# Performance work log

Hardware: AMD Instinct MI355X
Metric: run time of the kernel (lower is better)

## Reference

```python
import jax, jax.numpy as jnp
import numpy as np

N_NODES = 100000
N_EDGES = 1600000
IN_CH, HID1, HID2, HID3, OUT_CH = 128, 64, 64, 256, 64


def gcn_conv(x, W, b, src, dst, n_nodes):
    """PyG GCNConv: linear transform, add self-loops, symmetric-normalized aggregation."""
    h = x @ W  # [N, d_out]
    # degree at target nodes, counting the self-loop (+1)
    deg = jnp.zeros((n_nodes,), dtype=h.dtype).at[dst].add(1.0) + 1.0
    dinv = jax.lax.rsqrt(deg)  # deg >= 1, safe
    norm = dinv[src] * dinv[dst]  # [E]
    # scatter-add normalized messages from src to dst
    agg = jnp.zeros_like(h).at[dst].add(h[src] * norm[:, None])
    # self-loop contribution: norm_ii = dinv[i]^2
    agg = agg + h * (dinv * dinv)[:, None]
    return agg + b


def setup_inputs() -> dict:
    key = jax.random.key(0)
    ks = jax.random.split(key, 8)
    x = jax.random.normal(ks[0], (N_NODES, IN_CH), dtype=jnp.float32)
    edge_index = jax.random.randint(ks[1], (2, N_EDGES), 0, N_NODES, dtype=jnp.int64)
    def glorot(k, fan_in, fan_out):
        s = jnp.sqrt(6.0 / (fan_in + fan_out)).astype(jnp.float32)
        return jax.random.uniform(k, (fan_in, fan_out), jnp.float32, -s, s)
    return {
        "x": x,
        "edge_index": edge_index,
        "W1": glorot(ks[2], IN_CH, HID1), "b1": jnp.zeros((HID1,), jnp.float32),
        "W2": glorot(ks[3], HID1, HID2), "b2": jnp.zeros((HID2,), jnp.float32),
        "W3": glorot(ks[4], HID2, HID3), "b3": jnp.zeros((HID3,), jnp.float32),
        "W4": glorot(ks[5], HID3, OUT_CH), "b4": jnp.zeros((OUT_CH,), jnp.float32),
    }


def reference(x, edge_index, W1, b1, W2, b2, W3, b3, W4, b4):
    src, dst = edge_index[0], edge_index[1]
    n = x.shape[0]
    h = jax.nn.relu(gcn_conv(x, W1, b1, src, dst, n))
    h = jax.nn.relu(gcn_conv(h, W2, b2, src, dst, n))
    h = h @ W3 + b3  # hidden Linear (no activation, per original forward)
    h = h @ W4 + b4  # output Linear
    return jax.nn.log_softmax(h, axis=-1)
```

## Files before the change

kernel.cpp:

```cpp
#include <hip/hip_runtime.h>
#include <hip/hip_bf16.h>
#include <math.h>

#define NNODES 100000
#define NEDGES 1600000
#define NB 782
#define PB 256
#define EPB 6250
#define SCAN_N (NB * PB)
#define SB ((SCAN_N + 1023) / 1024)
#define CAP 4608
#define HTS 72
#define ANB 64

typedef __bf16 bf16x8 __attribute__((ext_vector_type(8)));
typedef float f32x4 __attribute__((ext_vector_type(4)));
typedef unsigned int u32x4 __attribute__((ext_vector_type(4)));
typedef unsigned short u16x8 __attribute__((ext_vector_type(8)));

static __device__ inline unsigned short f2bf(float f) {
    __hip_bfloat16 h = __float2bfloat16(f);
    return *reinterpret_cast<unsigned short*>(&h);
}


static __device__ inline int packidx64(int k, int ch) {
    int s = k >> 5, r5 = k & 31, q = r5 >> 3, ii = r5 & 7;
    int t = ch >> 4, lo = ch & 15;
    int lane = q * 16 + lo;
    return ((t * 2 + s) * 64 + lane) * 8 + ii;
}

__global__ __launch_bounds__(256) void histprep_kernel(const int* __restrict__ dst,
                                                       int* __restrict__ histg,
                                                       const float* __restrict__ W1,
                                                       const float* __restrict__ W2,
                                                       const float* __restrict__ W3,
                                                       const float* __restrict__ W4,
                                                       const float* __restrict__ b3,
                                                       const float* __restrict__ b4,
                                                       unsigned short* __restrict__ Wp1,
                                                       unsigned short* __restrict__ Wp2,
                                                       unsigned short* __restrict__ Wp34,
                                                       float* __restrict__ b34,
                                                       unsigned short* __restrict__ hp) {
    __shared__ int h[NB];
    int tid = threadIdx.x, blk = blockIdx.x;
    if (blk < PB) {
        for (int b = tid; b < NB; b += 256) h[b] = 0;
        __syncthreads();
        int base = blk * EPB;
        for (int i = base + tid; i < base + EPB; i += 256)
            atomicAdd(&h[dst[i] >> 7], 1);
        __syncthreads();
        for (int b = tid; b < NB; b += 256) histg[b * PB + blk] = h[b];
        return;
    }
    int pb = blk - PB;
    if (pb < 32) {
        int idx = pb * 256 + tid;
        int i = idx & 7, rest = idx >> 3;
        int lane = rest & 63; rest >>= 6;
        int s = rest % 4, t = rest / 4;
        int k = s * 32 + (lane >> 4) * 8 + i;
        int ch = t * 16 + (lane & 15);
        Wp1[idx] = f2bf(W1[k * 64 + ch]);
    } else if (pb < 48) {
        int idx = (pb - 32) * 256 + tid;
        int i = idx & 7, rest = idx >> 3;
        int lane = rest & 63; rest >>= 6;
        int s = rest % 2, t = rest / 2;
        int k = s * 32 + (lane >> 4) * 8 + i;
        int ch = t * 16 + (lane & 15);
        Wp2[idx] = f2bf(W2[k * 64 + ch]);
    } else if (pb == 48) {
        if (tid < 64) hp[(size_t)NNODES * 64 + tid] = 0;
    } else if (pb < 65) {
        int i = (pb - 49) * 4 + (tid >> 6);
        int j = tid & 63;
        float a = 0.f;
        for (int k = 0; k < 256; ++k) a = fmaf(W3[i * 256 + k], W4[k * 64 + j], a);
        Wp34[packidx64(i, j)] = f2bf(a);
    } else {
        if (tid < 64) {
            int j = tid;
            float a = b4[j];
            for (int k = 0; k < 256; ++k) a = fmaf(b3[k], W4[k * 64 + j], a);
            b34[j] = a;
        }
    }
}


__global__ __launch_bounds__(256) void scan1_kernel(const int* __restrict__ cnt,
                                                    int* __restrict__ off,
                                                    int* __restrict__ bsum, int n) {
    __shared__ int tmp[256];
    int tid = threadIdx.x;
    int t4 = blockIdx.x * 1024 + tid * 4;
    int v0 = (t4 + 0 < n) ? cnt[t4 + 0] : 0;
    int v1 = (t4 + 1 < n) ? cnt[t4 + 1] : 0;
    int v2 = (t4 + 2 < n) ? cnt[t4 + 2] : 0;
    int v3 = (t4 + 3 < n) ? cnt[t4 + 3] : 0;
    int ssum = v0 + v1 + v2 + v3;
    tmp[tid] = ssum;
    __syncthreads();
    for (int d = 1; d < 256; d <<= 1) {
        int x = (tid >= d) ? tmp[tid - d] : 0;
        __syncthreads();
        tmp[tid] += x;
        __syncthreads();
    }
    int run = tmp[tid] - ssum;
    if (t4 + 0 < n) off[t4 + 0] = run; run += v0;
    if (t4 + 1 < n) off[t4 + 1] = run; run += v1;
    if (t4 + 2 < n) off[t4 + 2] = run; run += v2;
    if (t4 + 3 < n) off[t4 + 3] = run;
    if (tid == 255) bsum[blockIdx.x] = tmp[255];
}


__global__ __launch_bounds__(256) void part_kernel(const int* __restrict__ src,
                                                   const int* __restrict__ dst,
                                                   const int* __restrict__ histg,
                                                   const int* __restrict__ gscan,
                                                   const int* __restrict__ bsum,
                                                   unsigned int* __restrict__ part) {
    __shared__ unsigned int sorted[EPB];
    __shared__ int gaddr[EPB];
    __shared__ int gcol[NB];
    __shared__ int base_l[NB];
    __shared__ int cur[NB];
    __shared__ int tmp[256];
    __shared__ int bse[256];
    int tid = threadIdx.x, blk = blockIdx.x;
    int bv = (tid < SB) ? bsum[tid] : 0;
    tmp[tid] = bv;
    __syncthreads();
    for (int d = 1; d < 256; d <<= 1) {
        int x = (tid >= d) ? tmp[tid - d] : 0;
        __syncthreads();
        tmp[tid] += x;
        __syncthreads();
    }
    bse[tid] = tmp[tid] - bv;
    __syncthreads();
    for (int b = tid; b < NB; b += 256) {
        int i = b * PB + blk;
        gcol[b] = gscan[i] + bse[i >> 10];
        base_l[b] = histg[i];
        cur[b] = 0;
    }
    __syncthreads();
    int t4 = tid * 4;
    int v0 = (t4 + 0 < NB) ? base_l[t4 + 0] : 0;
    int v1 = (t4 + 1 < NB) ? base_l[t4 + 1] : 0;
    int v2 = (t4 + 2 < NB) ? base_l[t4 + 2] : 0;
    int v3 = (t4 + 3 < NB) ? base_l[t4 + 3] : 0;
    int ssum = v0 + v1 + v2 + v3;
    tmp[tid] = ssum;
    __syncthreads();
    for (int d = 1; d < 256; d <<= 1) {
        int x = (tid >= d) ? tmp[tid - d] : 0;
        __syncthreads();
        tmp[tid] += x;
        __syncthreads();
    }
    int run = tmp[tid] - ssum;
    if (t4 + 0 < NB) base_l[t4 + 0] = run; run += v0;
    if (t4 + 1 < NB) base_l[t4 + 1] = run; run += v1;
    if (t4 + 2 < NB) base_l[t4 + 2] = run; run += v2;
    if (t4 + 3 < NB) base_l[t4 + 3] = run;
    __syncthreads();
    int base = blk * EPB;
    for (int i = base + tid; i < base + EPB; i += 256) {
        int s = src[i], d = dst[i];
        int bkt = d >> 7;
        int r = atomicAdd(&cur[bkt], 1);
        int pos = base_l[bkt] + r;
        sorted[pos] = ((unsigned int)(d & 127) << 17) | (unsigned int)s;
        gaddr[pos] = gcol[bkt] + r;
    }
    __syncthreads();
    for (int i = tid; i < EPB; i += 256)
        part[gaddr[i]] = sorted[i];
}


__global__ __launch_bounds__(256) void csrgemm_kernel(const unsigned int* __restrict__ part,
                                                      const int* __restrict__ gscan,
                                                      const int* __restrict__ bsum,
                                                      const float* __restrict__ x,
                                                      const unsigned short* __restrict__ Wp1,
                                                      int* __restrict__ csr,
                                                      int* __restrict__ cnt_g,
                                                      int* __restrict__ off_g,
                                                      float* __restrict__ dinv_g,
                                                      unsigned short* __restrict__ hp, int n) {
    __shared__ unsigned int stage[CAP];
    __shared__ int hist2[128];
    __shared__ int sc[128];
    __shared__ int excl[128];
    __shared__ int cur2[128];
    __shared__ float sdinv[128];
    __shared__ int tmp[256];
    __shared__ int bse[256];
    int tid = threadIdx.x, b = blockIdx.x;
    int bv = (tid < SB) ? bsum[tid] : 0;
    tmp[tid] = bv;
    __syncthreads();
    for (int d = 1; d < 256; d <<= 1) {
        int x2 = (tid >= d) ? tmp[tid - d] : 0;
        __syncthreads();
        tmp[tid] += x2;
        __syncthreads();
    }
    bse[tid] = tmp[tid] - bv;
    __syncthreads();
    int i0 = b * PB;
    int S = gscan[i0] + bse[i0 >> 10];
    int T = (b == NB - 1) ? NEDGES : (gscan[i0 + PB] + bse[(i0 + PB) >> 10]);
    int len = T - S;
    bool fit = (len <= CAP);
    if (tid < 128) { hist2[tid] = 0; cur2[tid] = 0; }
    __syncthreads();
    for (int i = tid; i < len; i += 256) {
        unsigned int p = part[S + i];
        if (fit) stage[i] = p;
        atomicAdd(&hist2[p >> 17], 1);
    }
    __syncthreads();
    if (tid < 128) sc[tid] = hist2[tid];
    __syncthreads();
    for (int d = 1; d < 128; d <<= 1) {
        int x2 = 0;
        if (tid < 128 && tid >= d) x2 = sc[tid - d];
        __syncthreads();
        if (tid < 128) sc[tid] += x2;
        __syncthreads();
    }
    if (tid < 128) {
        int c = hist2[tid];
        int ex = sc[tid] - c;
        excl[tid] = ex;
        float dv = rsqrtf((float)c + 1.0f);
        sdinv[tid] = dv;
        int node = b * 128 + tid;
        if (node < n) {
            cnt_g[node] = c;
            off_g[node] = S + ex;
            dinv_g[node] = dv;
        }
    }
    __syncthreads();
    for (int i = tid; i < len; i += 256) {
        unsigned int p = fit ? stage[i] : part[S + i];
        int dl = p >> 17;
        int s = (int)(p & 0x1FFFFu);
        int r = atomicAdd(&cur2[dl], 1);
        csr[S + excl[dl] + r] = s;
    }
    int wv = tid >> 6, lane = tid & 63;
    int q = lane >> 4, lo = lane & 15;
#pragma unroll
    for (int t2 = 0; t2 < 2; ++t2) {
        int nl0 = wv * 32 + t2 * 16;
        int nodeA = b * 128 + nl0 + lo;
        int na = nodeA < n ? nodeA : 0;
        f32x4 acc[4] = {};
#pragma unroll
        for (int s = 0; s < 4; ++s) {
            const float* xr = x + (size_t)na * 128 + q * 8 + s * 32;
            float4 u = *(const float4*)(xr);
            float4 v = *(const float4*)(xr + 4);
            bf16x8 a;
            a[0] = (__bf16)u.x; a[1] = (__bf16)u.y; a[2] = (__bf16)u.z; a[3] = (__bf16)u.w;
            a[4] = (__bf16)v.x; a[5] = (__bf16)v.y; a[6] = (__bf16)v.z; a[7] = (__bf16)v.w;
#pragma unroll
            for (int t = 0; t < 4; ++t) {
                bf16x8 bfr = *(const bf16x8*)(Wp1 + ((size_t)(t * 4 + s) * 64 + lane) * 8);
                acc[t] = __builtin_amdgcn_mfma_f32_16x16x32_bf16(a, bfr, acc[t], 0, 0, 0);
            }
        }
#pragma unroll
        for (int r = 0; r < 4; ++r) {
            int nl = nl0 + q * 4 + r;
            int node = b * 128 + nl;
            if (node < n) {
                float di = sdinv[nl];
#pragma unroll
                for (int t = 0; t < 4; ++t)
                    hp[(size_t)node * 64 + t * 16 + lo] = f2bf(acc[t][r] * di);
            }
        }
    }
}


template <bool LSM>
__global__ __launch_bounds__(256) void aggfuse_kernel(const unsigned short* __restrict__ hsrc,
                                                      const int* __restrict__ csr,
                                                      const int* __restrict__ off,
                                                      const int* __restrict__ cnt,
                                                      const float* __restrict__ dinv,
                                                      const float* __restrict__ biasA,
                                                      const unsigned short* __restrict__ Wp,
                                                      const float* __restrict__ biasB,
                                                      unsigned short* __restrict__ outb,
                                                      float* __restrict__ outf, int n) {
    __shared__ __align__(16) unsigned short ht[ANB * HTS];
    int tid = threadIdx.x, b = blockIdx.x;
    int g = tid >> 3, cl = tid & 7, c8 = cl * 8;
    float4 bv0 = *(const float4*)(biasA + c8);
    float4 bv1 = *(const float4*)(biasA + c8 + 4);
    float bb[8] = {bv0.x, bv0.y, bv0.z, bv0.w, bv1.x, bv1.y, bv1.z, bv1.w};
#pragma unroll 1
    for (int i = 0; i < 2; ++i) {
        int nl = g * 2 + i;
        int node = b * ANB + nl;
        u16x8 hv;
#pragma unroll
        for (int k = 0; k < 8; ++k) hv[k] = 0;
        if (node < n) {
            int s = off[node];
            int c = cnt[node];
            const int* cp = csr + s;
            float acc0[8];
            float acc1[8] = {};
            bf16x8 sv = *(const bf16x8*)(hsrc + (size_t)node * 64 + c8);
            u32x4 su = __builtin_bit_cast(u32x4, sv);
#pragma unroll
            for (int k = 0; k < 4; ++k) {
                acc0[2 * k]     = __builtin_bit_cast(float, su[k] << 16);
                acc0[2 * k + 1] = __builtin_bit_cast(float, su[k] & 0xFFFF0000u);
            }
            int n0 = 0, n1 = 0, n2 = 0, n3 = 0;
            if (c >= 4) { n0 = cp[0]; n1 = cp[1]; n2 = cp[2]; n3 = cp[3]; }
            int j = 0;
            for (; j + 4 <= c; j += 4) {
                bf16x8 va = *(const bf16x8*)(hsrc + (size_t)n0 * 64 + c8);
                bf16x8 vb = *(const bf16x8*)(hsrc + (size_t)n1 * 64 + c8);
                bf16x8 vc = *(const bf16x8*)(hsrc + (size_t)n2 * 64 + c8);
                bf16x8 vd = *(const bf16x8*)(hsrc + (size_t)n3 * 64 + c8);
                int jn = j + 4;
                if (jn + 4 <= c) { n0 = cp[jn]; n1 = cp[jn + 1]; n2 = cp[jn + 2]; n3 = cp[jn + 3]; }
                u32x4 ua = __builtin_bit_cast(u32x4, va);
                u32x4 ub = __builtin_bit_cast(u32x4, vb);
                u32x4 uc = __builtin_bit_cast(u32x4, vc);
                u32x4 ud = __builtin_bit_cast(u32x4, vd);
#pragma unroll
                for (int k = 0; k < 4; ++k) {
                    acc0[2 * k]     += __builtin_bit_cast(float, ua[k] << 16);
                    acc0[2 * k + 1] += __builtin_bit_cast(float, ua[k] & 0xFFFF0000u);
                    acc1[2 * k]     += __builtin_bit_cast(float, ub[k] << 16);
                    acc1[2 * k + 1] += __builtin_bit_cast(float, ub[k] & 0xFFFF0000u);
                    acc0[2 * k]     += __builtin_bit_cast(float, uc[k] << 16);
                    acc0[2 * k + 1] += __builtin_bit_cast(float, uc[k] & 0xFFFF0000u);
                    acc1[2 * k]     += __builtin_bit_cast(float, ud[k] << 16);
                    acc1[2 * k + 1] += __builtin_bit_cast(float, ud[k] & 0xFFFF0000u);
                }
            }
            for (; j < c; ++j) {
                int nt = cp[j];
                bf16x8 va = *(const bf16x8*)(hsrc + (size_t)nt * 64 + c8);
                u32x4 ua = __builtin_bit_cast(u32x4, va);
#pragma unroll
                for (int k = 0; k < 4; ++k) {
                    acc0[2 * k]     += __builtin_bit_cast(float, ua[k] << 16);
                    acc0[2 * k + 1] += __builtin_bit_cast(float, ua[k] & 0xFFFF0000u);
                }
            }
            float di = dinv[node];
#pragma unroll
            for (int k = 0; k < 8; ++k)
                hv[k] = f2bf(fmaxf(fmaf(acc0[k] + acc1[k], di, bb[k]), 0.f));
        }
        *(u16x8*)(&ht[nl * HTS + c8]) = hv;
    }
    __syncthreads();
    int wv = tid >> 6, lane = tid & 63;
    int q = lane >> 4, lo = lane & 15;
    int nl0 = wv * 16;
    f32x4 acc[4] = {};
#pragma unroll
    for (int s = 0; s < 2; ++s) {
        bf16x8 a = *(const bf16x8*)(&ht[(nl0 + lo) * HTS + s * 32 + q * 8]);
#pragma unroll
        for (int t = 0; t < 4; ++t) {
            bf16x8 bfr = *(const bf16x8*)(Wp + ((size_t)(t * 2 + s) * 64 + lane) * 8);
            acc[t] = __builtin_amdgcn_mfma_f32_16x16x32_bf16(a, bfr, acc[t], 0, 0, 0);
        }
    }
    if (!LSM) {
#pragma unroll
        for (int r = 0; r < 4; ++r) {
            int node = b * ANB + nl0 + q * 4 + r;
            if (node < n) {
                float di = dinv[node];
#pragma unroll
                for (int t = 0; t < 4; ++t)
                    outb[(size_t)node * 64 + t * 16 + lo] = f2bf(acc[t][r] * di);
            }
        }
    } else {
#pragma unroll
        for (int r = 0; r < 4; ++r) {
            int node = b * ANB + nl0 + q * 4 + r;
            float v0 = acc[0][r] + biasB[0 * 16 + lo];
            float v1 = acc[1][r] + biasB[1 * 16 + lo];
            float v2 = acc[2][r] + biasB[2 * 16 + lo];
            float v3 = acc[3][r] + biasB[3 * 16 + lo];
            float mx = fmaxf(fmaxf(v0, v1), fmaxf(v2, v3));
            for (int d = 1; d < 16; d <<= 1) mx = fmaxf(mx, __shfl_xor(mx, d));
            float sm = __expf(v0 - mx) + __expf(v1 - mx) + __expf(v2 - mx) + __expf(v3 - mx);
            for (int d = 1; d < 16; d <<= 1) sm += __shfl_xor(sm, d);
            float lse = mx + __logf(sm);
            if (node < n) {
                outf[(size_t)node * 64 + 0 * 16 + lo] = v0 - lse;
                outf[(size_t)node * 64 + 1 * 16 + lo] = v1 - lse;
                outf[(size_t)node * 64 + 2 * 16 + lo] = v2 - lse;
                outf[(size_t)node * 64 + 3 * 16 + lo] = v3 - lse;
            }
        }
    }
}


extern "C" void kernel_launch(void* const* d_in, const int* in_sizes, int n_in,
                              void* d_out, int out_size, void* d_ws, size_t ws_size,
                              hipStream_t stream) {
    const float* x  = (const float*)d_in[0];
    const int*   ei = (const int*)d_in[1];
    const float* W1 = (const float*)d_in[2];
    const float* b1 = (const float*)d_in[3];
    const float* W2 = (const float*)d_in[4];
    const float* b2 = (const float*)d_in[5];
    const float* W3 = (const float*)d_in[6];
    const float* b3 = (const float*)d_in[7];
    const float* W4 = (const float*)d_in[8];
    const float* b4 = (const float*)d_in[9];
    float* outp = (float*)d_out;

    const int N = NNODES;
    const int E = NEDGES;
    const int* srcp = ei;
    const int* dstp = ei + E;

    char* w = (char*)d_ws;
    size_t o = 0;
    auto alloc = [&](size_t bytes) { size_t r = o; o = (o + bytes + 255) & ~(size_t)255; return r; };
    size_t cnt_off   = alloc((size_t)N * 4);
    size_t off_off   = alloc((size_t)N * 4);
    size_t dinv_off  = alloc((size_t)N * 4);
    size_t histg_off = alloc((size_t)SCAN_N * 4);
    size_t gscan_off = alloc((size_t)SCAN_N * 4);
    size_t bs_off    = alloc(256 * 4);
    size_t part_off  = alloc((size_t)E * 4);
    size_t csr_off   = alloc((size_t)E * 4);
    size_t hp_off    = alloc((size_t)(N + 1) * 64 * 2);
    size_t abf_off   = alloc((size_t)N * 64 * 2);
    size_t wp1_off   = alloc(128 * 64 * 2);
    size_t wp2_off   = alloc(64 * 64 * 2);
    size_t wp34_off  = alloc(64 * 64 * 2);
    size_t b34_off   = alloc(64 * 4);

    int*            cnt   = (int*)(w + cnt_off);
    int*            off   = (int*)(w + off_off);
    float*          dinv  = (float*)(w + dinv_off);
    int*            histg = (int*)(w + histg_off);
    int*            gscan = (int*)(w + gscan_off);
    int*            bs    = (int*)(w + bs_off);
    unsigned int*   part  = (unsigned int*)(w + part_off);
    int*            csr   = (int*)(w + csr_off);
    unsigned short* hp    = (unsigned short*)(w + hp_off);
    unsigned short* abf   = (unsigned short*)(w + abf_off);
    unsigned short* Wp1   = (unsigned short*)(w + wp1_off);
    unsigned short* Wp2   = (unsigned short*)(w + wp2_off);
    unsigned short* Wp34  = (unsigned short*)(w + wp34_off);
    float*          b34   = (float*)(w + b34_off);

    histprep_kernel<<<PB + 66, 256, 0, stream>>>(dstp, histg, W1, W2, W3, W4, b3, b4,
                                                 Wp1, Wp2, Wp34, b34, hp);
    scan1_kernel<<<SB, 256, 0, stream>>>(histg, gscan, bs, SCAN_N);
    part_kernel<<<PB, 256, 0, stream>>>(srcp, dstp, histg, gscan, bs, part);
    csrgemm_kernel<<<NB, 256, 0, stream>>>(part, gscan, bs, x, Wp1, csr, cnt, off, dinv, hp, N);

    const int ab = (N + ANB - 1) / ANB;

    aggfuse_kernel<false><<<ab, 256, 0, stream>>>(hp, csr, off, cnt, dinv, b1, Wp2,
                                                  nullptr, abf, nullptr, N);
    aggfuse_kernel<true><<<ab, 256, 0, stream>>>(abf, csr, off, cnt, dinv, b2, Wp34,
                                                 b34, nullptr, outp, N);
}
```

Before: 245.0 us.

## Split fused aggregate-GEMM into column-sliced aggregation and separate GEMM kernels

```diff
diff --git a/kernel.cpp b/kernel.cpp
--- a/kernel.cpp
+++ b/kernel.cpp
@@ -10,13 +10,11 @@
 #define SCAN_N (NB * PB)
 #define SB ((SCAN_N + 1023) / 1024)
 #define CAP 4608
-#define HTS 72
-#define ANB 64
+#define NCH 391
 
 typedef __bf16 bf16x8 __attribute__((ext_vector_type(8)));
 typedef float f32x4 __attribute__((ext_vector_type(4)));
 typedef unsigned int u32x4 __attribute__((ext_vector_type(4)));
-typedef unsigned short u16x8 __attribute__((ext_vector_type(8)));
 
 static __device__ inline unsigned short f2bf(float f) {
     __hip_bfloat16 h = __float2bfloat16(f);
@@ -297,104 +295,100 @@
 }
 
 
+__global__ __launch_bounds__(256) void aggslice_kernel(const unsigned short* __restrict__ hsrc,
+                                                       const int* __restrict__ csr,
+                                                       const int* __restrict__ off,
+                                                       const int* __restrict__ cnt,
+                                                       const float* __restrict__ dinv,
+                                                       const float* __restrict__ bias,
+                                                       unsigned short* __restrict__ out, int n) {
+    int bid = blockIdx.x;
+    int chunk = bid >> 3, slice8 = (bid & 7) * 8;
+    int node = chunk * 256 + threadIdx.x;
+    if (node >= n) return;
+    const unsigned short* tab = hsrc + slice8;
+
+    int c = cnt[node];
+    int s = off[node];
+    const int* cp = csr + s;
+
+    float accA[8];
+    float accB[8] = {};
+    {
+        u32x4 su = *(const u32x4*)(tab + (size_t)node * 64);
+#pragma unroll
+        for (int k = 0; k < 4; ++k) {
+            accA[2 * k]     = __builtin_bit_cast(float, su[k] << 16);
+            accA[2 * k + 1] = __builtin_bit_cast(float, su[k] & 0xFFFF0000u);
+        }
+    }
+    int s0 = 0, s1 = 0;
+    if (c > 0) s0 = cp[0];
+    if (c > 1) s1 = cp[1];
+    int j = 0;
+    for (; j + 2 <= c; j += 2) {
+        u32x4 ua = *(const u32x4*)(tab + (size_t)s0 * 64);
+        u32x4 ub = *(const u32x4*)(tab + (size_t)s1 * 64);
+        if (j + 3 < c)      { s0 = cp[j + 2]; s1 = cp[j + 3]; }
+        else if (j + 2 < c) { s0 = cp[j + 2]; }
+#pragma unroll
+        for (int k = 0; k < 4; ++k) {
+            accA[2 * k]     += __builtin_bit_cast(float, ua[k] << 16);
+            accA[2 * k + 1] += __builtin_bit_cast(float, ua[k] & 0xFFFF0000u);
+            accB[2 * k]     += __builtin_bit_cast(float, ub[k] << 16);
+            accB[2 * k + 1] += __builtin_bit_cast(float, ub[k] & 0xFFFF0000u);
+        }
+    }
+    if (j < c) {
+        u32x4 ua = *(const u32x4*)(tab + (size_t)s0 * 64);
+#pragma unroll
+        for (int k = 0; k < 4; ++k) {
+            accA[2 * k]     += __builtin_bit_cast(float, ua[k] << 16);
+            accA[2 * k + 1] += __builtin_bit_cast(float, ua[k] & 0xFFFF0000u);
+        }
+    }
+
+    float di = dinv[node];
+    float4 bv0 = *(const float4*)(bias + slice8);
+    float4 bv1 = *(const float4*)(bias + slice8 + 4);
+    float bb[8] = {bv0.x, bv0.y, bv0.z, bv0.w, bv1.x, bv1.y, bv1.z, bv1.w};
+    unsigned short ov[8];
+#pragma unroll
+    for (int k = 0; k < 8; ++k)
+        ov[k] = f2bf(fmaxf(fmaf(accA[k] + accB[k], di, bb[k]), 0.f));
+    *(ushort4*)(out + (size_t)node * 64 + slice8)     = make_ushort4(ov[0], ov[1], ov[2], ov[3]);
+    *(ushort4*)(out + (size_t)node * 64 + slice8 + 4) = make_ushort4(ov[4], ov[5], ov[6], ov[7]);
+}
+
+
 template <bool LSM>
-__global__ __launch_bounds__(256) void aggfuse_kernel(const unsigned short* __restrict__ hsrc,
-                                                      const int* __restrict__ csr,
-                                                      const int* __restrict__ off,
-                                                      const int* __restrict__ cnt,
-                                                      const float* __restrict__ dinv,
-                                                      const float* __restrict__ biasA,
-                                                      const unsigned short* __restrict__ Wp,
-                                                      const float* __restrict__ biasB,
-                                                      unsigned short* __restrict__ outb,
-                                                      float* __restrict__ outf, int n) {
-    __shared__ __align__(16) unsigned short ht[ANB * HTS];
-    int tid = threadIdx.x, b = blockIdx.x;
-    int g = tid >> 3, cl = tid & 7, c8 = cl * 8;
-    float4 bv0 = *(const float4*)(biasA + c8);
-    float4 bv1 = *(const float4*)(biasA + c8 + 4);
-    float bb[8] = {bv0.x, bv0.y, bv0.z, bv0.w, bv1.x, bv1.y, bv1.z, bv1.w};
-#pragma unroll 1
-    for (int i = 0; i < 2; ++i) {
-        int nl = g * 2 + i;
-        int node = b * ANB + nl;
-        u16x8 hv;
-#pragma unroll
-        for (int k = 0; k < 8; ++k) hv[k] = 0;
-        if (node < n) {
-            int s = off[node];
-            int c = cnt[node];
-            const int* cp = csr + s;
-            float acc0[8];
-            float acc1[8] = {};
-            bf16x8 sv = *(const bf16x8*)(hsrc + (size_t)node * 64 + c8);
-            u32x4 su = __builtin_bit_cast(u32x4, sv);
-#pragma unroll
-            for (int k = 0; k < 4; ++k) {
-                acc0[2 * k]     = __builtin_bit_cast(float, su[k] << 16);
-                acc0[2 * k + 1] = __builtin_bit_cast(float, su[k] & 0xFFFF0000u);
-            }
-            int n0 = 0, n1 = 0, n2 = 0, n3 = 0;
-            if (c >= 4) { n0 = cp[0]; n1 = cp[1]; n2 = cp[2]; n3 = cp[3]; }
-            int j = 0;
-            for (; j + 4 <= c; j += 4) {
-                bf16x8 va = *(const bf16x8*)(hsrc + (size_t)n0 * 64 + c8);
-                bf16x8 vb = *(const bf16x8*)(hsrc + (size_t)n1 * 64 + c8);
-                bf16x8 vc = *(const bf16x8*)(hsrc + (size_t)n2 * 64 + c8);
-                bf16x8 vd = *(const bf16x8*)(hsrc + (size_t)n3 * 64 + c8);
-                int jn = j + 4;
-                if (jn + 4 <= c) { n0 = cp[jn]; n1 = cp[jn + 1]; n2 = cp[jn + 2]; n3 = cp[jn + 3]; }
-                u32x4 ua = __builtin_bit_cast(u32x4, va);
-                u32x4 ub = __builtin_bit_cast(u32x4, vb);
-                u32x4 uc = __builtin_bit_cast(u32x4, vc);
-                u32x4 ud = __builtin_bit_cast(u32x4, vd);
-#pragma unroll
-                for (int k = 0; k < 4; ++k) {
-                    acc0[2 * k]     += __builtin_bit_cast(float, ua[k] << 16);
-                    acc0[2 * k + 1] += __builtin_bit_cast(float, ua[k] & 0xFFFF0000u);
-                    acc1[2 * k]     += __builtin_bit_cast(float, ub[k] << 16);
-                    acc1[2 * k + 1] += __builtin_bit_cast(float, ub[k] & 0xFFFF0000u);
-                    acc0[2 * k]     += __builtin_bit_cast(float, uc[k] << 16);
-                    acc0[2 * k + 1] += __builtin_bit_cast(float, uc[k] & 0xFFFF0000u);
-                    acc1[2 * k]     += __builtin_bit_cast(float, ud[k] << 16);
-                    acc1[2 * k + 1] += __builtin_bit_cast(float, ud[k] & 0xFFFF0000u);
-                }
-            }
-            for (; j < c; ++j) {
-                int nt = cp[j];
-                bf16x8 va = *(const bf16x8*)(hsrc + (size_t)nt * 64 + c8);
-                u32x4 ua = __builtin_bit_cast(u32x4, va);
-#pragma unroll
-                for (int k = 0; k < 4; ++k) {
-                    acc0[2 * k]     += __builtin_bit_cast(float, ua[k] << 16);
-                    acc0[2 * k + 1] += __builtin_bit_cast(float, ua[k] & 0xFFFF0000u);
-                }
-            }
-            float di = dinv[node];
-#pragma unroll
-            for (int k = 0; k < 8; ++k)
-                hv[k] = f2bf(fmaxf(fmaf(acc0[k] + acc1[k], di, bb[k]), 0.f));
-        }
-        *(u16x8*)(&ht[nl * HTS + c8]) = hv;
-    }
-    __syncthreads();
-    int wv = tid >> 6, lane = tid & 63;
+__global__ __launch_bounds__(256) void gemm64_kernel(const unsigned short* __restrict__ Xb,
+                                                     const unsigned short* __restrict__ Wp,
+                                                     const float* __restrict__ biasB,
+                                                     const float* __restrict__ dinv,
+                                                     unsigned short* __restrict__ outb,
+                                                     float* __restrict__ outf, int n) {
+    int w = threadIdx.x >> 6, lane = threadIdx.x & 63;
     int q = lane >> 4, lo = lane & 15;
-    int nl0 = wv * 16;
+    int base = blockIdx.x * 64 + w * 16;
+    int nodeA = base + lo;
+    int na = nodeA < n ? nodeA : 0;
+
     f32x4 acc[4] = {};
 #pragma unroll
     for (int s = 0; s < 2; ++s) {
-        bf16x8 a = *(const bf16x8*)(&ht[(nl0 + lo) * HTS + s * 32 + q * 8]);
+        bf16x8 a = *(const bf16x8*)(Xb + (size_t)na * 64 + q * 8 + s * 32);
 #pragma unroll
         for (int t = 0; t < 4; ++t) {
-            bf16x8 bfr = *(const bf16x8*)(Wp + ((size_t)(t * 2 + s) * 64 + lane) * 8);
-            acc[t] = __builtin_amdgcn_mfma_f32_16x16x32_bf16(a, bfr, acc[t], 0, 0, 0);
-        }
-    }
+            bf16x8 b = *(const bf16x8*)(Wp + ((size_t)(t * 2 + s) * 64 + lane) * 8);
+            acc[t] = __builtin_amdgcn_mfma_f32_16x16x32_bf16(a, b, acc[t], 0, 0, 0);
+        }
+    }
+
     if (!LSM) {
 #pragma unroll
         for (int r = 0; r < 4; ++r) {
-            int node = b * ANB + nl0 + q * 4 + r;
+            int node = base + q * 4 + r;
             if (node < n) {
                 float di = dinv[node];
 #pragma unroll
@@ -405,7 +399,7 @@
     } else {
 #pragma unroll
         for (int r = 0; r < 4; ++r) {
-            int node = b * ANB + nl0 + q * 4 + r;
+            int node = base + q * 4 + r;
             float v0 = acc[0][r] + biasB[0 * 16 + lo];
             float v1 = acc[1][r] + biasB[1 * 16 + lo];
             float v2 = acc[2][r] + biasB[2 * 16 + lo];
@@ -485,10 +479,11 @@
     part_kernel<<<PB, 256, 0, stream>>>(srcp, dstp, histg, gscan, bs, part);
     csrgemm_kernel<<<NB, 256, 0, stream>>>(part, gscan, bs, x, Wp1, csr, cnt, off, dinv, hp, N);
 
-    const int ab = (N + ANB - 1) / ANB;
-
-    aggfuse_kernel<false><<<ab, 256, 0, stream>>>(hp, csr, off, cnt, dinv, b1, Wp2,
-                                                  nullptr, abf, nullptr, N);
-    aggfuse_kernel<true><<<ab, 256, 0, stream>>>(abf, csr, off, cnt, dinv, b2, Wp34,
-                                                 b34, nullptr, outp, N);
-}
+    const int ag = NCH * 8;
+    const int gb = (N + 63) / 64;
+
+    aggslice_kernel<<<ag, 256, 0, stream>>>(hp, csr, off, cnt, dinv, b1, abf, N);
+    gemm64_kernel<false><<<gb, 256, 0, stream>>>(abf, Wp2, nullptr, dinv, hp, nullptr, N);
+    aggslice_kernel<<<ag, 256, 0, stream>>>(hp, csr, off, cnt, dinv, b2, abf, N);
+    gemm64_kernel<true><<<gb, 256, 0, stream>>>(abf, Wp34, b34, nullptr, nullptr, outp, N);
+}
```

Result: slower. 664.1 us (+171.1%).

## Sort nodes by degree so aggregation blocks get balanced neighbor counts

Applied to the files above, without the earlier changes.

```diff
diff --git a/kernel.cpp b/kernel.cpp
--- a/kernel.cpp
+++ b/kernel.cpp
@@ -12,6 +12,7 @@
 #define CAP 4608
 #define HTS 72
 #define ANB 64
+#define DBINS 64
 
 typedef __bf16 bf16x8 __attribute__((ext_vector_type(8)));
 typedef float f32x4 __attribute__((ext_vector_type(4)));
@@ -43,7 +44,9 @@
                                                        unsigned short* __restrict__ Wp2,
                                                        unsigned short* __restrict__ Wp34,
                                                        float* __restrict__ b34,
-                                                       unsigned short* __restrict__ hp) {
+                                                       unsigned short* __restrict__ hp,
+                                                       int* __restrict__ dhist,
+                                                       int* __restrict__ gcur) {
     __shared__ int h[NB];
     int tid = threadIdx.x, blk = blockIdx.x;
     if (blk < PB) {
@@ -75,6 +78,7 @@
         Wp2[idx] = f2bf(W2[k * 64 + ch]);
     } else if (pb == 48) {
         if (tid < 64) hp[(size_t)NNODES * 64 + tid] = 0;
+        if (tid < DBINS) { dhist[tid] = 0; gcur[tid] = 0; }
     } else if (pb < 65) {
         int i = (pb - 49) * 4 + (tid >> 6);
         int j = tid & 63;
@@ -127,7 +131,7 @@
                                                    const int* __restrict__ bsum,
                                                    unsigned int* __restrict__ part) {
     __shared__ unsigned int sorted[EPB];
-    __shared__ int gaddr[EPB];
+    __shared__ unsigned short bktb[EPB];
     __shared__ int gcol[NB];
     __shared__ int base_l[NB];
     __shared__ int cur[NB];
@@ -179,11 +183,13 @@
         int r = atomicAdd(&cur[bkt], 1);
         int pos = base_l[bkt] + r;
         sorted[pos] = ((unsigned int)(d & 127) << 17) | (unsigned int)s;
-        gaddr[pos] = gcol[bkt] + r;
-    }
-    __syncthreads();
-    for (int i = tid; i < EPB; i += 256)
-        part[gaddr[i]] = sorted[i];
+        bktb[pos] = (unsigned short)bkt;
+    }
+    __syncthreads();
+    for (int i = tid; i < EPB; i += 256) {
+        int bkt = bktb[i];
+        part[gcol[bkt] + (i - base_l[bkt])] = sorted[i];
+    }
 }
 
 
@@ -196,7 +202,8 @@
                                                       int* __restrict__ cnt_g,
                                                       int* __restrict__ off_g,
                                                       float* __restrict__ dinv_g,
-                                                      unsigned short* __restrict__ hp, int n) {
+                                                      unsigned short* __restrict__ hp,
+                                                      int* __restrict__ dhist, int n) {
     __shared__ unsigned int stage[CAP];
     __shared__ int hist2[128];
     __shared__ int sc[128];
@@ -205,6 +212,7 @@
     __shared__ float sdinv[128];
     __shared__ int tmp[256];
     __shared__ int bse[256];
+    __shared__ int dh[DBINS];
     int tid = threadIdx.x, b = blockIdx.x;
     int bv = (tid < SB) ? bsum[tid] : 0;
     tmp[tid] = bv;
@@ -223,6 +231,7 @@
     int len = T - S;
     bool fit = (len <= CAP);
     if (tid < 128) { hist2[tid] = 0; cur2[tid] = 0; }
+    if (tid < DBINS) dh[tid] = 0;
     __syncthreads();
     for (int i = tid; i < len; i += 256) {
         unsigned int p = part[S + i];
@@ -250,9 +259,11 @@
             cnt_g[node] = c;
             off_g[node] = S + ex;
             dinv_g[node] = dv;
-        }
-    }
-    __syncthreads();
+            atomicAdd(&dh[c < 63 ? c : 63], 1);
+        }
+    }
+    __syncthreads();
+    if (tid < DBINS && dh[tid] > 0) atomicAdd(&dhist[tid], dh[tid]);
     for (int i = tid; i < len; i += 256) {
         unsigned int p = fit ? stage[i] : part[S + i];
         int dl = p >> 17;
@@ -293,6 +304,44 @@
                     hp[(size_t)node * 64 + t * 16 + lo] = f2bf(acc[t][r] * di);
             }
         }
+    }
+}
+
+
+__global__ __launch_bounds__(256) void permute_kernel(const int* __restrict__ cnt,
+                                                      const int* __restrict__ dhist,
+                                                      int* __restrict__ gcur,
+                                                      int* __restrict__ perm, int n) {
+    __shared__ int dbase[DBINS];
+    __shared__ int lh[DBINS];
+    __shared__ int lbase[DBINS];
+    __shared__ int lcur[DBINS];
+    __shared__ int sc[DBINS];
+    int tid = threadIdx.x;
+    int node = blockIdx.x * 256 + tid;
+    if (tid < DBINS) { sc[tid] = dhist[tid]; lh[tid] = 0; lcur[tid] = 0; }
+    __syncthreads();
+    for (int d = 1; d < DBINS; d <<= 1) {
+        int v = 0;
+        if (tid < DBINS && tid >= d) v = sc[tid - d];
+        __syncthreads();
+        if (tid < DBINS) sc[tid] += v;
+        __syncthreads();
+    }
+    if (tid < DBINS) dbase[tid] = sc[tid] - dhist[tid];
+    __syncthreads();
+    int bin = -1;
+    if (node < n) {
+        int c = cnt[node];
+        bin = c < 63 ? c : 63;
+        atomicAdd(&lh[bin], 1);
+    }
+    __syncthreads();
+    if (tid < DBINS && lh[tid] > 0) lbase[tid] = atomicAdd(&gcur[tid], lh[tid]);
+    __syncthreads();
+    if (node < n) {
+        int r = atomicAdd(&lcur[bin], 1);
+        perm[dbase[bin] + lbase[bin] + r] = node;
     }
 }
 
@@ -306,9 +355,11 @@
                                                       const float* __restrict__ biasA,
                                                       const unsigned short* __restrict__ Wp,
                                                       const float* __restrict__ biasB,
+                                                      const int* __restrict__ perm,
                                                       unsigned short* __restrict__ outb,
                                                       float* __restrict__ outf, int n) {
     __shared__ __align__(16) unsigned short ht[ANB * HTS];
+    __shared__ int pnode[ANB];
     int tid = threadIdx.x, b = blockIdx.x;
     int g = tid >> 3, cl = tid & 7, c8 = cl * 8;
     float4 bv0 = *(const float4*)(biasA + c8);
@@ -317,11 +368,13 @@
 #pragma unroll 1
     for (int i = 0; i < 2; ++i) {
         int nl = g * 2 + i;
-        int node = b * ANB + nl;
+        int slot = b * ANB + nl;
+        int node = (slot < n) ? perm[slot] : -1;
+        if (cl == 0) pnode[nl] = node;
         u16x8 hv;
 #pragma unroll
         for (int k = 0; k < 8; ++k) hv[k] = 0;
-        if (node < n) {
+        if (node >= 0) {
             int s = off[node];
             int c = cnt[node];
             const int* cp = csr + s;
@@ -394,8 +447,8 @@
     if (!LSM) {
 #pragma unroll
         for (int r = 0; r < 4; ++r) {
-            int node = b * ANB + nl0 + q * 4 + r;
-            if (node < n) {
+            int node = pnode[nl0 + q * 4 + r];
+            if (node >= 0) {
                 float di = dinv[node];
 #pragma unroll
                 for (int t = 0; t < 4; ++t)
@@ -405,7 +458,7 @@
     } else {
 #pragma unroll
         for (int r = 0; r < 4; ++r) {
-            int node = b * ANB + nl0 + q * 4 + r;
+            int node = pnode[nl0 + q * 4 + r];
             float v0 = acc[0][r] + biasB[0 * 16 + lo];
             float v1 = acc[1][r] + biasB[1 * 16 + lo];
             float v2 = acc[2][r] + biasB[2 * 16 + lo];
@@ -415,7 +468,7 @@
             float sm = __expf(v0 - mx) + __expf(v1 - mx) + __expf(v2 - mx) + __expf(v3 - mx);
             for (int d = 1; d < 16; d <<= 1) sm += __shfl_xor(sm, d);
             float lse = mx + __logf(sm);
-            if (node < n) {
+            if (node >= 0) {
                 outf[(size_t)node * 64 + 0 * 16 + lo] = v0 - lse;
                 outf[(size_t)node * 64 + 1 * 16 + lo] = v1 - lse;
                 outf[(size_t)node * 64 + 2 * 16 + lo] = v2 - lse;
@@ -452,9 +505,12 @@
     size_t cnt_off   = alloc((size_t)N * 4);
     size_t off_off   = alloc((size_t)N * 4);
     size_t dinv_off  = alloc((size_t)N * 4);
+    size_t perm_off  = alloc((size_t)N * 4);
     size_t histg_off = alloc((size_t)SCAN_N * 4);
     size_t gscan_off = alloc((size_t)SCAN_N * 4);
     size_t bs_off    = alloc(256 * 4);
+    size_t dh_off    = alloc(DBINS * 4);
+    size_t gc_off    = alloc(DBINS * 4);
     size_t part_off  = alloc((size_t)E * 4);
     size_t csr_off   = alloc((size_t)E * 4);
     size_t hp_off    = alloc((size_t)(N + 1) * 64 * 2);
@@ -467,9 +523,12 @@
     int*            cnt   = (int*)(w + cnt_off);
     int*            off   = (int*)(w + off_off);
     float*          dinv  = (float*)(w + dinv_off);
+    int*            perm  = (int*)(w + perm_off);
     int*            histg = (int*)(w + histg_off);
     int*            gscan = (int*)(w + gscan_off);
     int*            bs    = (int*)(w + bs_off);
+    int*            dhist = (int*)(w + dh_off);
+    int*            gcur  = (int*)(w + gc_off);
     unsigned int*   part  = (unsigned int*)(w + part_off);
     int*            csr   = (int*)(w + csr_off);
     unsigned short* hp    = (unsigned short*)(w + hp_off);
@@ -480,15 +539,18 @@
     float*          b34   = (float*)(w + b34_off);
 
     histprep_kernel<<<PB + 66, 256, 0, stream>>>(dstp, histg, W1, W2, W3, W4, b3, b4,
-                                                 Wp1, Wp2, Wp34, b34, hp);
+                                                 Wp1, Wp2, Wp34, b34, hp, dhist, gcur);
     scan1_kernel<<<SB, 256, 0, stream>>>(histg, gscan, bs, SCAN_N);
     part_kernel<<<PB, 256, 0, stream>>>(srcp, dstp, histg, gscan, bs, part);
-    csrgemm_kernel<<<NB, 256, 0, stream>>>(part, gscan, bs, x, Wp1, csr, cnt, off, dinv, hp, N);
+    csrgemm_kernel<<<NB, 256, 0, stream>>>(part, gscan, bs, x, Wp1, csr, cnt, off, dinv, hp, dhist, N);
+
+    const int pg = (N + 255) / 256;
+    permute_kernel<<<pg, 256, 0, stream>>>(cnt, dhist, gcur, perm, N);
 
     const int ab = (N + ANB - 1) / ANB;
 
     aggfuse_kernel<false><<<ab, 256, 0, stream>>>(hp, csr, off, cnt, dinv, b1, Wp2,
-                                                  nullptr, abf, nullptr, N);
+                                                  nullptr, perm, abf, nullptr, N);
     aggfuse_kernel<true><<<ab, 256, 0, stream>>>(abf, csr, off, cnt, dinv, b2, Wp34,
-                                                 b34, nullptr, outp, N);
-}
+                                                 b34, perm, nullptr, outp, N);
+}
```

Result: slower. 264.5 us (+8.0%).

## Balance per-node aggregation work by degree sort and shrink partition scratch

Applied to the files above, without the earlier changes.

```diff
diff --git a/kernel.cpp b/kernel.cpp
--- a/kernel.cpp
+++ b/kernel.cpp
@@ -127,7 +127,7 @@
                                                    const int* __restrict__ bsum,
                                                    unsigned int* __restrict__ part) {
     __shared__ unsigned int sorted[EPB];
-    __shared__ int gaddr[EPB];
+    __shared__ unsigned short bktb[EPB];
     __shared__ int gcol[NB];
     __shared__ int base_l[NB];
     __shared__ int cur[NB];
@@ -179,11 +179,13 @@
         int r = atomicAdd(&cur[bkt], 1);
         int pos = base_l[bkt] + r;
         sorted[pos] = ((unsigned int)(d & 127) << 17) | (unsigned int)s;
-        gaddr[pos] = gcol[bkt] + r;
-    }
-    __syncthreads();
-    for (int i = tid; i < EPB; i += 256)
-        part[gaddr[i]] = sorted[i];
+        bktb[pos] = (unsigned short)bkt;
+    }
+    __syncthreads();
+    for (int i = tid; i < EPB; i += 256) {
+        int bkt = bktb[i];
+        part[gcol[bkt] + (i - base_l[bkt])] = sorted[i];
+    }
 }
 
 
@@ -309,14 +311,32 @@
                                                       unsigned short* __restrict__ outb,
                                                       float* __restrict__ outf, int n) {
     __shared__ __align__(16) unsigned short ht[ANB * HTS];
+    __shared__ int sdeg[ANB];
+    __shared__ unsigned char sord[ANB];
     int tid = threadIdx.x, b = blockIdx.x;
     int g = tid >> 3, cl = tid & 7, c8 = cl * 8;
+    if (tid < ANB) {
+        int node = b * ANB + tid;
+        sdeg[tid] = (node < n) ? cnt[node] : -1;
+    }
+    __syncthreads();
+    if (tid < ANB) {
+        int d = sdeg[tid];
+        int r = 0;
+#pragma unroll 8
+        for (int j = 0; j < ANB; ++j) {
+            int dj = sdeg[j];
+            r += (dj > d) || (dj == d && j < tid);
+        }
+        sord[r] = (unsigned char)tid;
+    }
+    __syncthreads();
     float4 bv0 = *(const float4*)(biasA + c8);
     float4 bv1 = *(const float4*)(biasA + c8 + 4);
     float bb[8] = {bv0.x, bv0.y, bv0.z, bv0.w, bv1.x, bv1.y, bv1.z, bv1.w};
 #pragma unroll 1
     for (int i = 0; i < 2; ++i) {
-        int nl = g * 2 + i;
+        int nl = sord[i == 0 ? g : (ANB - 1 - g)];
         int node = b * ANB + nl;
         u16x8 hv;
 #pragma unroll
```

Result: no change. 249.0 us, median of 2 (+1.7%).
